# Optimization experiments

Hardware: AMD Instinct MI355X
Metric: run time of the kernel (lower is better)

## Reference

```python
import jax, jax.numpy as jnp
import numpy as np

DECAY = 0.99
EPS = 1e-05


def setup_inputs() -> dict:
    key = jax.random.key(0)
    k1, k2, k3, k4 = jax.random.split(key, 4)
    x = jax.random.normal(k1, (32, 64, 64, 64), jnp.float32)          # [B,H,W,dim]
    embed = jax.random.normal(k2, (64, 1024), jnp.float32)            # [dim, n_embed] buffer
    cluster_size = jax.random.uniform(k3, (1024,), jnp.float32)       # EMA cluster-size buffer
    embed_avg = jax.random.normal(k4, (64, 1024), jnp.float32)        # EMA embed-avg buffer
    return {"x": x, "embed": embed, "cluster_size": cluster_size, "embed_avg": embed_avg}


def reference(x, embed, cluster_size, embed_avg):
    dim = x.shape[-1]
    n_embed = embed.shape[1]
    flatten = x.reshape(-1, dim)                                      # [N, dim]
    # squared distances: ||f||^2 - 2 f.E + ||e||^2   -> [N, n_embed]
    dist = ((flatten * flatten).sum(1, keepdims=True)
            - 2.0 * (flatten @ embed)
            + (embed * embed).sum(0, keepdims=True))
    idx = jnp.argmin(dist, axis=1)                                    # [N]
    quantize = jnp.take(embed.T, idx, axis=0).reshape(x.shape)        # codebook gather
    embed_ind = idx.reshape(x.shape[:-1])

    # EMA codebook update (training branch); stats detached as in torch (buffers, .data ops)
    fl = jax.lax.stop_gradient(flatten)
    onehot_sum = jax.ops.segment_sum(jnp.ones_like(idx, dtype=x.dtype), idx, num_segments=n_embed)
    embed_sum = jax.ops.segment_sum(fl, idx, num_segments=n_embed).T  # [dim, n_embed]
    new_cluster_size = DECAY * cluster_size + (1.0 - DECAY) * onehot_sum
    new_embed_avg = DECAY * embed_avg + (1.0 - DECAY) * embed_sum
    n = new_cluster_size.sum()
    cs = (new_cluster_size + EPS) / (n + n_embed * EPS) * n
    new_embed = new_embed_avg / cs[None, :]

    diff = jnp.mean((jax.lax.stop_gradient(quantize) - x) ** 2)       # commitment loss
    quantize_st = x + jax.lax.stop_gradient(quantize - x)             # straight-through
    return (quantize_st, diff, embed_ind, new_cluster_size, new_embed_avg, new_embed)
```

## Files before the change

kernel.cpp:

```cpp
#include <hip/hip_runtime.h>


#define N_ROWS 131072
#define DIM    64
#define NEMB   1024
#define FLAG_CAP 131072
#define TAU 0.02f
#define NRANGE 32

static constexpr float DECAYF = 0.99f;
static constexpr float OMDF   = (float)(1.0 - 0.99);
static constexpr float EPSF   = 1e-5f;
static constexpr float NEPSF  = (float)(1024 * 1e-5);

typedef __attribute__((ext_vector_type(8))) short short8;
typedef __attribute__((ext_vector_type(4))) float f32x4;

static __device__ __forceinline__ unsigned short f2bf(float f) {
    unsigned int u = __builtin_bit_cast(unsigned int, f);
    unsigned int r = (u + 0x7FFFu + ((u >> 16) & 1u)) >> 16;
    return (unsigned short)r;
}
static __device__ __forceinline__ float bf2f(unsigned short h) {
    unsigned int u = ((unsigned int)h) << 16;
    return __builtin_bit_cast(float, u);
}

#define WS_ESUM    0
#define WS_CNTF    65536
#define WS_DIFF    66560
#define WS_FLAGCNT 66561
#define WS_N       66562
#define WS_EE      66564
#define WS_EMBEDT  67588
#define WS_IDX     133124
#define WS_FLAGLST 264196
#define WS_BFRAG   395268
#define WS_CNTPART 460804
#define WS_PART    493572
#define WS_NEED_BYTES ((size_t)(WS_PART + NRANGE * 65536) * 4)

__global__ void prep_kernel(const float* __restrict__ embed,
                            float* __restrict__ embedT,
                            float* __restrict__ ee,
                            uint4* __restrict__ BfragG) {
    int tid = blockIdx.x * 256 + threadIdx.x;
    for (int i = 0; i < 4; ++i) {
        int id = i * 16384 + tid;
        int d = id >> 10, e = id & 1023;
        embedT[e * 64 + d] = embed[id];
    }
    if (tid < NEMB) {
        float s = 0.f;
        for (int d = 0; d < DIM; ++d) {
            float v = embed[d * 1024 + tid];
            s = fmaf(v, v, s);
        }
        ee[tid] = s;
    }
    int fid  = tid >> 6;
    int lane = tid & 63;
    int hl = fid & 1, kt = (fid >> 1) & 1, ct = fid >> 2;
    int col = ct * 16 + (lane & 15);
    int k0  = kt * 32 + (lane >> 4) * 8;
    unsigned short u[8];
    #pragma unroll
    for (int j = 0; j < 8; ++j) {
        float v = -2.0f * embed[(k0 + j) * 1024 + col];
        unsigned short h = f2bf(v);
        if (hl) h = f2bf(v - bf2f(h));
        u[j] = h;
    }
    uint4 wv;
    wv.x = (unsigned)u[0] | ((unsigned)u[1] << 16);
    wv.y = (unsigned)u[2] | ((unsigned)u[3] << 16);
    wv.z = (unsigned)u[4] | ((unsigned)u[5] << 16);
    wv.w = (unsigned)u[6] | ((unsigned)u[7] << 16);
    BfragG[fid * 64 + lane] = wv;
}

__global__ __launch_bounds__(256) void dist_kernel(
        const float* __restrict__ x, const uint4* __restrict__ BfragG,
        const float* __restrict__ ee, const float* __restrict__ embedT,
        float* __restrict__ out_q, float* __restrict__ out_ind,
        int* __restrict__ ws_idx, float* __restrict__ ws_diff,
        int* __restrict__ ws_flagcnt, int* __restrict__ ws_flaglist) {
    __shared__ uint4 Bs[2048];
    __shared__ int   sIdx[128];
    __shared__ float red[4];

    const int t = threadIdx.x;
    const int w = t >> 6, lane = t & 63;
    const int quad = lane >> 4, wl = lane & 15;
    const int rbase = blockIdx.x * 128;

    short8 a_hi[2][2], a_lo[2][2];
    #pragma unroll
    for (int rt = 0; rt < 2; ++rt) {
        int row = rbase + w * 32 + rt * 16 + wl;
        #pragma unroll
        for (int kt = 0; kt < 2; ++kt) {
            const float* px = x + (size_t)row * 64 + kt * 32 + quad * 8;
            float4 v0 = *(const float4*)px;
            float4 v1 = *(const float4*)(px + 4);
            float vv[8] = {v0.x, v0.y, v0.z, v0.w, v1.x, v1.y, v1.z, v1.w};
            short8 ah, al;
            #pragma unroll
            for (int j = 0; j < 8; ++j) {
                unsigned short h = f2bf(vv[j]);
                ah[j] = (short)h;
                al[j] = (short)f2bf(vv[j] - bf2f(h));
            }
            a_hi[rt][kt] = ah; a_lo[rt][kt] = al;
        }
    }

    float b1[8], b2[8];
    int   i1[8];
    #pragma unroll
    for (int s = 0; s < 8; ++s) { b1[s] = 3.4e38f; b2[s] = 3.4e38f; i1[s] = 0; }

    const f32x4 zacc = {0.f, 0.f, 0.f, 0.f};

    for (int ch = 0; ch < 8; ++ch) {
        __syncthreads();
        const uint4* src = BfragG + ch * 2048;
        #pragma unroll
        for (int it = 0; it < 8; ++it) Bs[it * 256 + t] = src[it * 256 + t];
        __syncthreads();

        #pragma unroll
        for (int ctl = 0; ctl < 8; ++ctl) {
            const short8* bp = (const short8*)Bs;
            short8 bh0 = bp[(ctl * 4 + 0) * 64 + lane];
            short8 bl0 = bp[(ctl * 4 + 1) * 64 + lane];
            short8 bh1 = bp[(ctl * 4 + 2) * 64 + lane];
            short8 bl1 = bp[(ctl * 4 + 3) * 64 + lane];
            int col = ch * 128 + ctl * 16 + wl;
            float eec = ee[col];
            #pragma unroll
            for (int rt = 0; rt < 2; ++rt) {
                f32x4 c0 = __builtin_amdgcn_mfma_f32_16x16x32_bf16(a_lo[rt][0], bh0, zacc, 0, 0, 0);
                f32x4 c1 = __builtin_amdgcn_mfma_f32_16x16x32_bf16(a_lo[rt][1], bh1, zacc, 0, 0, 0);
                c0 = __builtin_amdgcn_mfma_f32_16x16x32_bf16(a_hi[rt][0], bl0, c0, 0, 0, 0);
                c1 = __builtin_amdgcn_mfma_f32_16x16x32_bf16(a_hi[rt][1], bl1, c1, 0, 0, 0);
                c0 = __builtin_amdgcn_mfma_f32_16x16x32_bf16(a_hi[rt][0], bh0, c0, 0, 0, 0);
                c1 = __builtin_amdgcn_mfma_f32_16x16x32_bf16(a_hi[rt][1], bh1, c1, 0, 0, 0);
                #pragma unroll
                for (int reg = 0; reg < 4; ++reg) {
                    float s = c0[reg] + c1[reg] + eec;
                    int st = rt * 4 + reg;
                    bool lt = s < b1[st];
                    b2[st] = fminf(fmaxf(s, b1[st]), b2[st]);
                    i1[st] = lt ? col : i1[st];
                    b1[st] = fminf(s, b1[st]);
                }
            }
        }
    }

    for (int m = 1; m < 16; m <<= 1) {
        #pragma unroll
        for (int s = 0; s < 8; ++s) {
            float ob1 = __shfl_xor(b1[s], m);
            int   oi1 = __shfl_xor(i1[s], m);
            float ob2 = __shfl_xor(b2[s], m);
            if (ob1 < b1[s] || (ob1 == b1[s] && oi1 < i1[s])) {
                b2[s] = fminf(b1[s], ob2); b1[s] = ob1; i1[s] = oi1;
            } else {
                b2[s] = fminf(b2[s], ob1);
            }
        }
    }
    if (wl == 0) {
        #pragma unroll
        for (int s = 0; s < 8; ++s) {
            int rt = s >> 2, reg = s & 3;
            int rloc = w * 32 + rt * 16 + quad * 4 + reg;
            int row = rbase + rloc;
            sIdx[rloc] = i1[s];
            ws_idx[row] = i1[s];
            out_ind[row] = (float)i1[s];
            if (b2[s] - b1[s] < TAU) {
                int pos = atomicAdd(ws_flagcnt, 1);
                if (pos < FLAG_CAP) ws_flaglist[pos] = row;
            }
        }
    }
    __syncthreads();

    {
        int r = t >> 1, hh = t & 1;
        int e = sIdx[r];
        const float4* et = (const float4*)(embedT + e * 64 + hh * 32);
        const float4* xr = (const float4*)(x + (size_t)(rbase + r) * 64 + hh * 32);
        float4*       qo = (float4*)(out_q + (size_t)(rbase + r) * 64 + hh * 32);
        float dsum = 0.f;
        #pragma unroll
        for (int v = 0; v < 8; ++v) {
            float4 q4 = et[v];
            float4 x4 = xr[v];
            float dx = q4.x - x4.x, dy = q4.y - x4.y, dz = q4.z - x4.z, dw = q4.w - x4.w;
            float4 o;
            o.x = x4.x + dx; o.y = x4.y + dy; o.z = x4.z + dz; o.w = x4.w + dw;
            qo[v] = o;
            dsum += dx * dx + dy * dy + dz * dz + dw * dw;
        }
        for (int o2 = 32; o2 > 0; o2 >>= 1) dsum += __shfl_down(dsum, o2);
        if (lane == 0) red[w] = dsum;
        __syncthreads();
        if (t == 0) atomicAdd(ws_diff, red[0] + red[1] + red[2] + red[3]);
    }
}

__global__ __launch_bounds__(256) void recheck_kernel(
        const float* __restrict__ x, const float* __restrict__ embed,
        const float* __restrict__ embedT, const float* __restrict__ ee,
        const int* __restrict__ flagcnt, const int* __restrict__ flaglist,
        int* __restrict__ ws_idx, float* __restrict__ out_ind,
        float* __restrict__ out_q, float* __restrict__ ws_diff) {
    __shared__ float sx[8][64];
    __shared__ float sff[8];
    __shared__ int   srow[8];
    __shared__ float sbd[256];
    __shared__ int   sbi[256];
    __shared__ int   schg[2];
    int t = threadIdx.x;
    int cnt = *flagcnt;
    if (cnt > FLAG_CAP) cnt = FLAG_CAP;
    int ntiles = (cnt + 7) >> 3;
    for (int tile = blockIdx.x; tile < ntiles; tile += gridDim.x) {
        int base = tile * 8;
        int nr = cnt - base; if (nr > 8) nr = 8;
        __syncthreads();
        if (t < nr) srow[t] = flaglist[base + t];
        __syncthreads();
        for (int l = t; l < nr * 64; l += 256)
            sx[l >> 6][l & 63] = x[(size_t)srow[l >> 6] * 64 + (l & 63)];
        __syncthreads();
        if (t < nr) {
            float ff = 0.f;
            for (int k = 0; k < 64; ++k) ff = fmaf(sx[t][k], sx[t][k], ff);
            sff[t] = ff;
        }
        float acc[8][4];
        #pragma unroll
        for (int r = 0; r < 8; ++r)
            #pragma unroll
            for (int j = 0; j < 4; ++j) acc[r][j] = 0.f;
        int c0 = t * 4;
        for (int k = 0; k < 64; ++k) {
            float4 e4 = *(const float4*)(embed + k * 1024 + c0);
            #pragma unroll
            for (int r = 0; r < 8; ++r) {
                float xk = sx[r][k];
                acc[r][0] = fmaf(xk, e4.x, acc[r][0]);
                acc[r][1] = fmaf(xk, e4.y, acc[r][1]);
                acc[r][2] = fmaf(xk, e4.z, acc[r][2]);
                acc[r][3] = fmaf(xk, e4.w, acc[r][3]);
            }
        }
        __syncthreads();
        for (int r = 0; r < nr; ++r) {
            int row = srow[r];
            float ff = sff[r];
            float bd = 3.4e38f; int bi = 0;
            #pragma unroll
            for (int j = 0; j < 4; ++j) {
                float d = (ff - 2.f * acc[r][j]) + ee[c0 + j];
                if (d < bd) { bd = d; bi = c0 + j; }
            }
            sbd[t] = bd; sbi[t] = bi;
            __syncthreads();
            for (int s = 128; s > 0; s >>= 1) {
                if (t < s) {
                    float od = sbd[t + s]; int oi = sbi[t + s];
                    if (od < sbd[t] || (od == sbd[t] && oi < sbi[t])) { sbd[t] = od; sbi[t] = oi; }
                }
                __syncthreads();
            }
            if (t == 0) {
                int ni = sbi[0], oi = ws_idx[row];
                schg[0] = ni; schg[1] = oi;
                if (ni != oi) { ws_idx[row] = ni; out_ind[row] = (float)ni; }
            }
            __syncthreads();
            int ni = schg[0], oi = schg[1];
            if (ni != oi && t < 64) {
                float xv = sx[r][t];
                float dn = embedT[ni * 64 + t] - xv;
                float dold = embedT[oi * 64 + t] - xv;
                out_q[(size_t)row * 64 + t] = xv + dn;
                float delta = dn * dn - dold * dold;
                for (int o = 32; o > 0; o >>= 1) delta += __shfl_down(delta, o);
                if (t == 0) atomicAdd(ws_diff, delta);
            }
            __syncthreads();
        }
    }
}

__global__ __launch_bounds__(256) void scatter_kernel(
        const int* __restrict__ idx, const float* __restrict__ x,
        float* __restrict__ part_or_esum, float* __restrict__ cntp_or_cntf,
        int use_atomic) {
    __shared__ float shist[8192];
    __shared__ float scnt[1024];
    const int t = threadIdx.x;
    const int rb = blockIdx.x >> 3, oct = blockIdx.x & 7;
    const int w = t >> 6, lane = t & 63;
    const int g = lane >> 3, d = lane & 7;

    for (int i = t; i < 8192; i += 256) shist[i] = 0.f;
    if (oct == 0) for (int i = t; i < 1024; i += 256) scnt[i] = 0.f;
    __syncthreads();

    const int row0 = rb * 4096 + w * 1024;
    int rcur = row0 + g;
    int e_n = idx[rcur];
    float x_n = x[(size_t)rcur * 64 + oct * 8 + d];
    for (int it = 0; it < 128; ++it) {
        int e = e_n; float xv = x_n;
        int rnext = rcur + 8;
        if (it < 127) {
            e_n = idx[rnext];
            x_n = x[(size_t)rnext * 64 + oct * 8 + d];
        }
        rcur = rnext;
        atomicAdd(&shist[d * 1024 + e], xv);
        if (oct == 0 && d == 0) atomicAdd(&scnt[e], 1.0f);
    }
    __syncthreads();

    if (!use_atomic) {
        float* dst = part_or_esum + (size_t)blockIdx.x * 8192;
        for (int cell = t; cell < 8192; cell += 256) dst[cell] = shist[cell];
        if (oct == 0) {
            float* cdst = cntp_or_cntf + rb * 1024;
            for (int i = t; i < 1024; i += 256) cdst[i] = scnt[i];
        }
    } else {
        for (int cell = t; cell < 8192; cell += 256) {
            float v = shist[cell];
            if (v != 0.f)
                atomicAdd(&part_or_esum[(oct * 8 + (cell >> 10)) * 1024 + (cell & 1023)], v);
        }
        if (oct == 0) {
            for (int i = t; i < 1024; i += 256) {
                float c = scnt[i];
                if (c != 0.f) atomicAdd(&cntp_or_cntf[i], c);
            }
        }
    }
}

__global__ __launch_bounds__(1024) void finalize1(
        const float* __restrict__ cluster_size, const float* __restrict__ cntp,
        int nrb, const float* __restrict__ ws_diff, float* __restrict__ out_diff,
        float* __restrict__ out_ncs, float* __restrict__ ws_n) {
    int t = threadIdx.x;
    float c = 0.f;
    for (int k = 0; k < nrb; ++k) c += cntp[k * 1024 + t];
    float ncs = DECAYF * cluster_size[t] + OMDF * c;
    out_ncs[t] = ncs;
    __shared__ float sred[16];
    float v = ncs;
    for (int o = 32; o > 0; o >>= 1) v += __shfl_down(v, o);
    if ((t & 63) == 0) sred[t >> 6] = v;
    __syncthreads();
    if (t == 0) {
        float n = 0.f;
        for (int i = 0; i < 16; ++i) n += sred[i];
        ws_n[0] = n;
        out_diff[0] = ws_diff[0] * (1.0f / 8388608.0f);
    }
}

__global__ __launch_bounds__(256) void finalize2(
        const float* __restrict__ embed_avg, const float* __restrict__ part,
        int nrb, const float* __restrict__ out_ncs, const float* __restrict__ ws_n,
        float* __restrict__ out_nea, float* __restrict__ out_ne) {
    int j = blockIdx.x * 256 + threadIdx.x;
    float es = 0.f;
    for (int k = 0; k < nrb; ++k) es += part[(size_t)k * 65536 + j];
    float n = ws_n[0];
    float nea = DECAYF * embed_avg[j] + OMDF * es;
    out_nea[j] = nea;
    float ncs = out_ncs[j & 1023];
    float cs = (ncs + EPSF) / (n + NEPSF) * n;
    out_ne[j] = nea / cs;
}

extern "C" void kernel_launch(void* const* d_in, const int* in_sizes, int n_in,
                              void* d_out, int out_size, void* d_ws, size_t ws_size,
                              hipStream_t stream) {
    const float* x            = (const float*)d_in[0];
    const float* embed        = (const float*)d_in[1];
    const float* cluster_size = (const float*)d_in[2];
    const float* embed_avg    = (const float*)d_in[3];

    float* out = (float*)d_out;
    float* out_q    = out;
    float* out_diff = out + 8388608;
    float* out_ind  = out + 8388609;
    float* out_ncs  = out + 8519681;
    float* out_nea  = out + 8520705;
    float* out_ne   = out + 8586241;

    float* ws = (float*)d_ws;
    float* ws_esum     = ws + WS_ESUM;
    float* ws_cntf     = ws + WS_CNTF;
    float* ws_diff     = ws + WS_DIFF;
    int*   ws_flagcnt  = (int*)(ws + WS_FLAGCNT);
    float* ws_n        = ws + WS_N;
    float* ws_ee       = ws + WS_EE;
    float* ws_embedT   = ws + WS_EMBEDT;
    int*   ws_idx      = (int*)(ws + WS_IDX);
    int*   ws_flaglist = (int*)(ws + WS_FLAGLST);
    uint4* ws_Bfrag    = (uint4*)(ws + WS_BFRAG);
    float* ws_cntpart  = ws + WS_CNTPART;
    float* ws_part     = ws + WS_PART;

    const int use_part = (ws_size >= WS_NEED_BYTES) ? 1 : 0;

    if (use_part) {
        hipMemsetAsync(ws + WS_DIFF, 0, 8, stream);
    } else {
        hipMemsetAsync(d_ws, 0, (size_t)(WS_FLAGCNT + 1) * 4, stream);
    }

    prep_kernel<<<64, 256, 0, stream>>>(embed, ws_embedT, ws_ee, ws_Bfrag);
    dist_kernel<<<N_ROWS / 128, 256, 0, stream>>>(x, ws_Bfrag, ws_ee, ws_embedT,
                                                  out_q, out_ind, ws_idx, ws_diff,
                                                  ws_flagcnt, ws_flaglist);
    recheck_kernel<<<256, 256, 0, stream>>>(x, embed, ws_embedT, ws_ee,
                                            ws_flagcnt, ws_flaglist,
                                            ws_idx, out_ind, out_q, ws_diff);
    scatter_kernel<<<NRANGE * 8, 256, 0, stream>>>(
        ws_idx, x,
        use_part ? ws_part : ws_esum,
        use_part ? ws_cntpart : ws_cntf,
        use_part ? 0 : 1);
    finalize1<<<1, 1024, 0, stream>>>(cluster_size,
                                      use_part ? ws_cntpart : ws_cntf,
                                      use_part ? NRANGE : 1,
                                      ws_diff, out_diff, out_ncs, ws_n);
    finalize2<<<256, 256, 0, stream>>>(embed_avg,
                                       use_part ? ws_part : ws_esum,
                                       use_part ? NRANGE : 1,
                                       out_ncs, ws_n, out_nea, out_ne);
}
```

Measured before the change: 283.8 us.

## Double-buffer codebook fragments via direct global-to-LDS loads; parallelize recheck argmin reduction

The distance kernel now stages codebook MFMA fragments in two 16KB LDS buffers using global_load_lds, prefetching the next chunk while computing the current one. It also caches the ee norms in shared memory instead of reading them from global each iteration. The recheck kernel replaces its serial per-row block-wide tree reduction, which had many __syncthreads, with wave-per-row shuffle reductions, and launches twice as many blocks. Risks are the hand-written vmcnt waits and barrier correctness, plus higher LDS use in recheck (16KB for sbd/sbi).

```diff
diff --git a/kernel.cpp b/kernel.cpp
--- a/kernel.cpp
+++ b/kernel.cpp
@@ -24,6 +24,12 @@
 static __device__ __forceinline__ float bf2f(unsigned short h) {
     unsigned int u = ((unsigned int)h) << 16;
     return __builtin_bit_cast(float, u);
+}
+
+static __device__ __forceinline__ void glds16(const uint4* g, uint4* l) {
+    __builtin_amdgcn_global_load_lds(
+        (const __attribute__((address_space(1))) unsigned int*)(g),
+        (__attribute__((address_space(3))) unsigned int*)(l), 16, 0, 0);
 }
 
 #define WS_ESUM    0
@@ -85,7 +91,8 @@
         float* __restrict__ out_q, float* __restrict__ out_ind,
         int* __restrict__ ws_idx, float* __restrict__ ws_diff,
         int* __restrict__ ws_flagcnt, int* __restrict__ ws_flaglist) {
-    __shared__ uint4 Bs[2048];
+    __shared__ uint4 Bs[2][1024];
+    __shared__ float sEE[1024];
     __shared__ int   sIdx[128];
     __shared__ float red[4];
 
@@ -115,6 +122,8 @@
         }
     }
 
+    for (int i = t; i < 1024; i += 256) sEE[i] = ee[i];
+
     float b1[8], b2[8];
     int   i1[8];
     #pragma unroll
@@ -122,22 +131,39 @@
 
     const f32x4 zacc = {0.f, 0.f, 0.f, 0.f};
 
-    for (int ch = 0; ch < 8; ++ch) {
-        __syncthreads();
-        const uint4* src = BfragG + ch * 2048;
-        #pragma unroll
-        for (int it = 0; it < 8; ++it) Bs[it * 256 + t] = src[it * 256 + t];
-        __syncthreads();
-
-        #pragma unroll
-        for (int ctl = 0; ctl < 8; ++ctl) {
-            const short8* bp = (const short8*)Bs;
+    __syncthreads();
+
+#define STAGE(chv, bv)                                                     \
+    {                                                                      \
+        const uint4* _src = BfragG + (chv) * 1024 + w * 256 + lane;        \
+        uint4* _dst = &Bs[bv][w * 256];                                    \
+        glds16(_src,       _dst);                                          \
+        glds16(_src + 64,  _dst + 64);                                     \
+        glds16(_src + 128, _dst + 128);                                    \
+        glds16(_src + 192, _dst + 192);                                    \
+    }
+
+    int buf = 0;
+    STAGE(0, 0);
+    for (int ch = 0; ch < 16; ++ch) {
+        if (ch < 15) {
+            STAGE(ch + 1, buf ^ 1);
+            asm volatile("s_waitcnt vmcnt(4)" ::: "memory");
+        } else {
+            asm volatile("s_waitcnt vmcnt(0)" ::: "memory");
+        }
+        __builtin_amdgcn_s_barrier();
+        asm volatile("" ::: "memory");
+
+        const short8* bp = (const short8*)&Bs[buf][0];
+        #pragma unroll
+        for (int ctl = 0; ctl < 4; ++ctl) {
             short8 bh0 = bp[(ctl * 4 + 0) * 64 + lane];
             short8 bl0 = bp[(ctl * 4 + 1) * 64 + lane];
             short8 bh1 = bp[(ctl * 4 + 2) * 64 + lane];
             short8 bl1 = bp[(ctl * 4 + 3) * 64 + lane];
-            int col = ch * 128 + ctl * 16 + wl;
-            float eec = ee[col];
+            int col = ch * 64 + ctl * 16 + wl;
+            float eec = sEE[col];
             #pragma unroll
             for (int rt = 0; rt < 2; ++rt) {
                 f32x4 c0 = __builtin_amdgcn_mfma_f32_16x16x32_bf16(a_lo[rt][0], bh0, zacc, 0, 0, 0);
@@ -157,7 +183,11 @@
                 }
             }
         }
-    }
+        asm volatile("s_waitcnt lgkmcnt(0)" ::: "memory");
+        __builtin_amdgcn_s_barrier();
+        buf ^= 1;
+    }
+#undef STAGE
 
     for (int m = 1; m < 16; m <<= 1) {
         #pragma unroll
@@ -222,10 +252,10 @@
     __shared__ float sx[8][64];
     __shared__ float sff[8];
     __shared__ int   srow[8];
-    __shared__ float sbd[256];
-    __shared__ int   sbi[256];
-    __shared__ int   schg[2];
-    int t = threadIdx.x;
+    __shared__ float sbd[8][256];
+    __shared__ int   sbi[8][256];
+    const int t = threadIdx.x;
+    const int w = t >> 6, lane = t & 63;
     int cnt = *flagcnt;
     if (cnt > FLAG_CAP) cnt = FLAG_CAP;
     int ntiles = (cnt + 7) >> 3;
@@ -261,8 +291,8 @@
             }
         }
         __syncthreads();
-        for (int r = 0; r < nr; ++r) {
-            int row = srow[r];
+        #pragma unroll
+        for (int r = 0; r < 8; ++r) {
             float ff = sff[r];
             float bd = 3.4e38f; int bi = 0;
             #pragma unroll
@@ -270,32 +300,41 @@
                 float d = (ff - 2.f * acc[r][j]) + ee[c0 + j];
                 if (d < bd) { bd = d; bi = c0 + j; }
             }
-            sbd[t] = bd; sbi[t] = bi;
-            __syncthreads();
-            for (int s = 128; s > 0; s >>= 1) {
-                if (t < s) {
-                    float od = sbd[t + s]; int oi = sbi[t + s];
-                    if (od < sbd[t] || (od == sbd[t] && oi < sbi[t])) { sbd[t] = od; sbi[t] = oi; }
+            sbd[r][t] = bd; sbi[r][t] = bi;
+        }
+        __syncthreads();
+        #pragma unroll
+        for (int rr = 0; rr < 2; ++rr) {
+            int r = w * 2 + rr;
+            if (r < nr) {
+                float bd = sbd[r][lane]; int bi = sbi[r][lane];
+                #pragma unroll
+                for (int k2 = 1; k2 < 4; ++k2) {
+                    float od = sbd[r][lane + 64 * k2];
+                    int   oi = sbi[r][lane + 64 * k2];
+                    if (od < bd || (od == bd && oi < bi)) { bd = od; bi = oi; }
                 }
-                __syncthreads();
-            }
-            if (t == 0) {
-                int ni = sbi[0], oi = ws_idx[row];
-                schg[0] = ni; schg[1] = oi;
-                if (ni != oi) { ws_idx[row] = ni; out_ind[row] = (float)ni; }
-            }
-            __syncthreads();
-            int ni = schg[0], oi = schg[1];
-            if (ni != oi && t < 64) {
-                float xv = sx[r][t];
-                float dn = embedT[ni * 64 + t] - xv;
-                float dold = embedT[oi * 64 + t] - xv;
-                out_q[(size_t)row * 64 + t] = xv + dn;
-                float delta = dn * dn - dold * dold;
-                for (int o = 32; o > 0; o >>= 1) delta += __shfl_down(delta, o);
-                if (t == 0) atomicAdd(ws_diff, delta);
-            }
-            __syncthreads();
+                for (int m = 32; m > 0; m >>= 1) {
+                    float od = __shfl_xor(bd, m);
+                    int   oi = __shfl_xor(bi, m);
+                    if (od < bd || (od == bd && oi < bi)) { bd = od; bi = oi; }
+                }
+                int row = srow[r];
+                int oi_old = ws_idx[row];
+                if (bi != oi_old) {
+                    float xv = sx[r][lane];
+                    float dn   = embedT[bi * 64 + lane] - xv;
+                    float dold = embedT[oi_old * 64 + lane] - xv;
+                    out_q[(size_t)row * 64 + lane] = xv + dn;
+                    float delta = dn * dn - dold * dold;
+                    for (int o = 32; o > 0; o >>= 1) delta += __shfl_down(delta, o);
+                    if (lane == 0) {
+                        ws_idx[row] = bi;
+                        out_ind[row] = (float)bi;
+                        atomicAdd(ws_diff, delta);
+                    }
+                }
+            }
         }
     }
 }
@@ -433,7 +472,7 @@
     dist_kernel<<<N_ROWS / 128, 256, 0, stream>>>(x, ws_Bfrag, ws_ee, ws_embedT,
                                                   out_q, out_ind, ws_idx, ws_diff,
                                                   ws_flagcnt, ws_flaglist);
-    recheck_kernel<<<256, 256, 0, stream>>>(x, embed, ws_embedT, ws_ee,
+    recheck_kernel<<<512, 256, 0, stream>>>(x, embed, ws_embedT, ws_ee,
                                             ws_flagcnt, ws_flaglist,
                                             ws_idx, out_ind, out_q, ws_diff);
     scatter_kernel<<<NRANGE * 8, 256, 0, stream>>>(
```

Result: no change. 286.7 us (+1.0%).
